# Kernel optimization log

Hardware: AMD Instinct MI355X
Metric: run time of the kernel (lower is better)

## Reference

```python
import jax, jax.numpy as jnp
import numpy as np

N = 100000
E = 3200000
FIRE, WEA, TER = 8, 12, 10
H = 64


def setup_inputs() -> dict:
    key = jax.random.key(0)
    ks = jax.random.split(key, 24)
    def lin(kw, fan_in, fan_out):
        # torch nn.Linear default init: U(-1/sqrt(fan_in), 1/sqrt(fan_in))
        b = 1.0 / np.sqrt(fan_in)
        W = jax.random.uniform(kw, (fan_in, fan_out), jnp.float32, -b, b)
        return W
    inp = {
        'x_fire': jax.random.normal(ks[0], (N, FIRE), jnp.float32),
        'x_weather': jax.random.normal(ks[1], (N, WEA), jnp.float32),
        'x_terrain': jax.random.normal(ks[2], (N, TER), jnp.float32),
        'edge_index': jax.random.randint(ks[3], (2, E), 0, N, jnp.int64),
        # modality encoders
        'w_fire': lin(ks[4], FIRE, H), 'b_fire': jnp.zeros((H,), jnp.float32),
        'w_wea': lin(ks[5], WEA, H),  'b_wea': jnp.zeros((H,), jnp.float32),
        'w_ter': lin(ks[6], TER, H),  'b_ter': jnp.zeros((H,), jnp.float32),
        # GCN layers (concat fusion -> first layer in_dim = 3H)
        'gcn_w0': lin(ks[7], 3 * H, H), 'gcn_b0': jnp.zeros((H,), jnp.float32),
        'gcn_w1': lin(ks[8], H, H),     'gcn_b1': jnp.zeros((H,), jnp.float32),
        'gcn_w2': lin(ks[9], H, H),     'gcn_b2': jnp.zeros((H,), jnp.float32),
        # output MLP: H -> H//2 -> 1
        'out_w1': lin(ks[10], H, H // 2), 'out_b1': jnp.zeros((H // 2,), jnp.float32),
        'out_w2': lin(ks[11], H // 2, 1), 'out_b2': jnp.zeros((1,), jnp.float32),
    }
    return inp


def _gcn_conv(x, src, dst, W, b):
    """PyG GCNConv: h = W x; out[i] = sum_{j->i} norm_ij h[j] + self-loop + bias,
    with norm_ij = deg[i]^-1/2 * deg[j]^-1/2, deg including the added self-loop."""
    h = x @ W                                             # [N, H]
    deg = jnp.zeros((N,), h.dtype).at[dst].add(1.0) + 1.0  # +1 self-loop
    dinv = jax.lax.rsqrt(deg)                             # deg^-0.5
    norm = dinv[src] * dinv[dst]                          # [E]
    agg = jnp.zeros_like(h).at[dst].add(h[src] * norm[:, None])
    agg = agg + h * (dinv * dinv)[:, None]                # self-loop contribution
    return agg + b


def reference(x_fire, x_weather, x_terrain, edge_index,
              w_fire, b_fire, w_wea, b_wea, w_ter, b_ter,
              gcn_w0, gcn_b0, gcn_w1, gcn_b1, gcn_w2, gcn_b2,
              out_w1, out_b1, out_w2, out_b2):
    # modality encoders (eval mode: dropout is identity)
    h_fire = jax.nn.relu(x_fire @ w_fire + b_fire)
    h_wea = jax.nn.relu(x_weather @ w_wea + b_wea)
    h_ter = jax.nn.relu(x_terrain @ w_ter + b_ter)
    x = jnp.concatenate([h_fire, h_wea, h_ter], axis=1)   # [N, 3H]
    src, dst = edge_index[0], edge_index[1]
    x = jax.nn.relu(_gcn_conv(x, src, dst, gcn_w0, gcn_b0))
    x = jax.nn.relu(_gcn_conv(x, src, dst, gcn_w1, gcn_b1))
    x = jax.nn.relu(_gcn_conv(x, src, dst, gcn_w2, gcn_b2))
    out = jax.nn.relu(x @ out_w1 + out_b1) @ out_w2 + out_b2
    return out
```

## Files before the change

### kernel.cpp

```cpp
#include <hip/hip_runtime.h>

#define NN 100000
#define NE 3200000
#define HD 64

#define NBUCK 256
#define BWID 392
#define SLACK 20480
#define COLCAP 13568
#define OVFCAP 512
#define CAP 16
#define P1_EPB 2048
#define P1_GRID ((NE + P1_EPB - 1) / P1_EPB)

typedef int      v4i __attribute__((ext_vector_type(4)));
typedef int      v2i __attribute__((ext_vector_type(2)));
typedef _Float16 h4f __attribute__((ext_vector_type(4)));

__device__ __forceinline__ void fma4(float4& a, float s, const float4& b) {
    a.x = fmaf(s, b.x, a.x); a.y = fmaf(s, b.y, a.y);
    a.z = fmaf(s, b.z, a.z); a.w = fmaf(s, b.w, a.w);
}
__device__ __forceinline__ void addh4(float4& a, const h4f& b) {
    a.x += (float)b[0]; a.y += (float)b[1]; a.z += (float)b[2]; a.w += (float)b[3];
}

__global__ void __launch_bounds__(256) partition_kernel(
    const int* __restrict__ src, const int* __restrict__ dst,
    int* __restrict__ bctl, v2i* __restrict__ pairs, v2i* __restrict__ povf) {
    __shared__ v2i stage[NBUCK][CAP];
    __shared__ int cnt[NBUCK];
    int t = threadIdx.x;
    cnt[t] = 0;
    __syncthreads();
    const v4i* d4p = (const v4i*)dst;
    const v4i* s4p = (const v4i*)src;
    const int NE4 = NE / 4;
    int base4 = blockIdx.x * (P1_EPB / 4);
    #pragma unroll
    for (int it = 0; it < P1_EPB / 1024; it++) {
        int i = base4 + it * 256 + t;
        v4i d4 = (v4i){-1, -1, -1, -1};
        v4i s4 = (v4i){0, 0, 0, 0};
        if (i < NE4) {
            d4 = __builtin_nontemporal_load(d4p + i);
            s4 = __builtin_nontemporal_load(s4p + i);
        }
        #pragma unroll
        for (int k = 0; k < 4; k++) {
            int d = d4[k];
            if (d >= 0) {
                int b = (unsigned)d / BWID;
                int slot = atomicAdd(&cnt[b], 1);
                v2i p; p[0] = s4[k]; p[1] = d;
                if (slot < CAP) {
                    stage[b][slot] = p;
                } else {
                    int o = atomicAdd(&bctl[b * 16 + 2], 1);
                    if (o < OVFCAP) povf[(size_t)b * OVFCAP + o] = p;
                }
            }
        }
    }
    __syncthreads();
    int c_tot = cnt[t];
    int c = (c_tot > CAP) ? CAP : c_tot;
    int runs = (c + 7) >> 3;
    if (runs) {
        int slots = runs * 8;
        for (int m = c; m < slots; m++) { v2i p; p[0] = 0; p[1] = -1; stage[t][m] = p; }
        int gb = atomicAdd(&bctl[t * 16], slots);
        if (gb + slots <= SLACK) {
            v4i* gp = (v4i*)(pairs + (size_t)t * SLACK + gb);
            const v4i* sp = (const v4i*)&stage[t][0];
            #pragma unroll
            for (int m = 0; m < 8; m++) { if (m < runs * 4) gp[m] = sp[m]; }
        } else {
            for (int m = 0; m < slots && gb + m < SLACK; m++)
                pairs[(size_t)t * SLACK + gb + m] = stage[t][m];
        }
    }
    if (c_tot > 0) atomicAdd(&bctl[t * 16 + 1], c_tot);
}

__global__ void bucket_scan_kernel(const int* __restrict__ bctl,
                                   int* __restrict__ bbase, int* __restrict__ rowptr) {
    __shared__ int s[NBUCK];
    int t = threadIdx.x;
    int v = bctl[t * 16 + 1];
    s[t] = v; __syncthreads();
    for (int off = 1; off < NBUCK; off <<= 1) {
        int x = (t >= off) ? s[t - off] : 0;
        __syncthreads();
        s[t] += x;
        __syncthreads();
    }
    bbase[t] = s[t] - v;
    if (t == NBUCK - 1) rowptr[NN] = s[t];
}

__global__ void __launch_bounds__(256) csr_fill_kernel(
    const v2i* __restrict__ pairs, const v2i* __restrict__ povf,
    const int* __restrict__ bctl, const int* __restrict__ bbase,
    int* __restrict__ rowptr, float* __restrict__ dinv, int* __restrict__ col) {
    __shared__ int hist[BWID];
    __shared__ int rp[BWID];
    __shared__ int cur[BWID];
    __shared__ int sc[256];
    __shared__ int cols[COLCAP];
    int b = blockIdx.x, t = threadIdx.x;
    int lo = b * BWID;
    int hi = min(lo + BWID, NN);
    int nw = hi - lo;
    for (int i = t; i < BWID; i += 256) { hist[i] = 0; cur[i] = 0; }
    __syncthreads();
    int np = bctl[b * 16];     if (np > SLACK) np = SLACK;
    int nov = bctl[b * 16 + 2]; if (nov > OVFCAP) nov = OVFCAP;
    int base = bbase[b];
    const v2i* pb = pairs + (size_t)b * SLACK;
    const v2i* ob = povf + (size_t)b * OVFCAP;
    for (int i = t; i < np; i += 256) {
        v2i p = pb[i];
        if (p[1] >= 0) atomicAdd(&hist[p[1] - lo], 1);
    }
    for (int i = t; i < nov; i += 256) {
        v2i p = ob[i];
        atomicAdd(&hist[p[1] - lo], 1);
    }
    __syncthreads();
    int h0 = 0, s2 = 0;
    if (2 * t < BWID) {
        h0 = hist[2 * t];
        int h1 = (2 * t + 1 < BWID) ? hist[2 * t + 1] : 0;
        s2 = h0 + h1;
    }
    sc[t] = s2; __syncthreads();
    for (int off = 1; off < 256; off <<= 1) {
        int x = (t >= off) ? sc[t - off] : 0;
        __syncthreads();
        sc[t] += x;
        __syncthreads();
    }
    if (2 * t < BWID) {
        int ex = sc[t] - s2;
        rp[2 * t] = ex;
        if (2 * t + 1 < BWID) rp[2 * t + 1] = ex + h0;
    }
    __syncthreads();
    for (int i = t; i < nw; i += 256) {
        rowptr[lo + i] = base + rp[i];
        dinv[lo + i] = 1.0f / sqrtf((float)(hist[i] + 1));
    }
    for (int i = t; i < np; i += 256) {
        v2i p = pb[i];
        if (p[1] >= 0) {
            int li = p[1] - lo;
            int slot = atomicAdd(&cur[li], 1);
            int o = rp[li] + slot;
            if (o < COLCAP) cols[o] = p[0];
        }
    }
    for (int i = t; i < nov; i += 256) {
        v2i p = ob[i];
        int li = p[1] - lo;
        int slot = atomicAdd(&cur[li], 1);
        int o = rp[li] + slot;
        if (o < COLCAP) cols[o] = p[0];
    }
    __syncthreads();
    int nreal = bctl[b * 16 + 1]; if (nreal > COLCAP) nreal = COLCAP;
    for (int i = t; i < nreal; i += 256)
        col[base + i] = cols[i];
}

__global__ void __launch_bounds__(256) encmm0_kernel(
    const float* __restrict__ xf, const float* __restrict__ xw, const float* __restrict__ xt,
    const float* __restrict__ Wf, const float* __restrict__ bf,
    const float* __restrict__ Ww, const float* __restrict__ bw,
    const float* __restrict__ Wt, const float* __restrict__ bt,
    const float* __restrict__ W0, const float* __restrict__ dinv,
    _Float16* __restrict__ h) {
    __shared__ float xin[64][32];
    __shared__ float wenc[30][64];
    __shared__ float bs[192];
    __shared__ float xs[64][36];
    __shared__ float ws[32][64];
    int t = threadIdx.x;
    int n0 = blockIdx.x * 64;

    {
        const float4* xf4 = (const float4*)xf;
        for (int i = t; i < 128; i += 256) {
            int n = i >> 1, q = i & 1;
            int gn = n0 + n;
            float4 v = make_float4(0, 0, 0, 0);
            if (gn < NN) v = xf4[(size_t)gn * 2 + q];
            *(float4*)&xin[n][q * 4] = v;
        }
        const float4* xw4 = (const float4*)xw;
        for (int i = t; i < 192; i += 256) {
            int n = i / 3, q = i - n * 3;
            int gn = n0 + n;
            float4 v = make_float4(0, 0, 0, 0);
            if (gn < NN) v = xw4[(size_t)gn * 3 + q];
            *(float4*)&xin[n][8 + q * 4] = v;
        }
        const float2* xt2 = (const float2*)xt;
        for (int i = t; i < 320; i += 256) {
            int n = i / 5, q = i - n * 5;
            int gn = n0 + n;
            float2 v = make_float2(0, 0);
            if (gn < NN) v = xt2[(size_t)gn * 5 + q];
            *(float2*)&xin[n][20 + q * 2] = v;
        }
        for (int i = t; i < 480; i += 256) {
            int r = i >> 4, q = i & 15;
            float4 v;
            if (r < 8)       v = ((const float4*)Wf)[r * 16 + q];
            else if (r < 20) v = ((const float4*)Ww)[(r - 8) * 16 + q];
            else             v = ((const float4*)Wt)[(r - 20) * 16 + q];
            *(float4*)&wenc[r][q * 4] = v;
        }
        if (t < 192) bs[t] = (t < 64) ? bf[t] : (t < 128) ? bw[t - 64] : bt[t - 128];
    }

    int cg = t & 15, ng = t >> 4;
    int c0 = cg * 4;
    float4 acc[4];
    #pragma unroll
    for (int i = 0; i < 4; i++) acc[i] = make_float4(0, 0, 0, 0);

    for (int kq = 0; kq < 6; kq++) {
        __syncthreads();
        {
            const float4* W04 = (const float4*)W0;
            float4* ws4 = (float4*)&ws[0][0];
            for (int i = t; i < 512; i += 256)
                ws4[i] = W04[(size_t)kq * 512 + i];
        }
        int coff = (kq < 2) ? kq * 32 : (kq < 4) ? (kq - 2) * 32 : (kq - 4) * 32;
        if (kq < 2) {
            for (int i = t; i < 2048; i += 256) {
                int n = i >> 5, kk = i & 31;
                float a = bs[kq * 32 + kk];
                #pragma unroll
                for (int k = 0; k < 8; k++) a = fmaf(xin[n][k], wenc[k][coff + kk], a);
                xs[n][kk] = fmaxf(a, 0.f);
            }
        } else if (kq < 4) {
            for (int i = t; i < 2048; i += 256) {
                int n = i >> 5, kk = i & 31;
                float a = bs[kq * 32 + kk];
                #pragma unroll
                for (int k = 0; k < 12; k++) a = fmaf(xin[n][8 + k], wenc[8 + k][coff + kk], a);
                xs[n][kk] = fmaxf(a, 0.f);
            }
        } else {
            for (int i = t; i < 2048; i += 256) {
                int n = i >> 5, kk = i & 31;
                float a = bs[kq * 32 + kk];
                #pragma unroll
                for (int k = 0; k < 10; k++) a = fmaf(xin[n][20 + k], wenc[20 + k][coff + kk], a);
                xs[n][kk] = fmaxf(a, 0.f);
            }
        }
        __syncthreads();
        for (int k = 0; k < 32; k += 4) {
            float4 b0 = *(const float4*)&ws[k + 0][c0];
            float4 b1 = *(const float4*)&ws[k + 1][c0];
            float4 b2 = *(const float4*)&ws[k + 2][c0];
            float4 b3 = *(const float4*)&ws[k + 3][c0];
            #pragma unroll
            for (int i = 0; i < 4; i++) {
                float4 a = *(const float4*)&xs[ng * 4 + i][k];
                fma4(acc[i], a.x, b0); fma4(acc[i], a.y, b1);
                fma4(acc[i], a.z, b2); fma4(acc[i], a.w, b3);
            }
        }
    }
    h4f* h4 = (h4f*)h;
    #pragma unroll
    for (int i = 0; i < 4; i++) {
        int gn = n0 + ng * 4 + i;
        if (gn < NN) {
            float dn = dinv[gn];
            h4f v;
            v[0] = (_Float16)(acc[i].x * dn);
            v[1] = (_Float16)(acc[i].y * dn);
            v[2] = (_Float16)(acc[i].z * dn);
            v[3] = (_Float16)(acc[i].w * dn);
            h4[(size_t)gn * 16 + cg] = v;
        }
    }
}

__global__ void gather_mm_kernel(
    const int* __restrict__ col, const int* __restrict__ rowptr,
    const float* __restrict__ dinv, const _Float16* __restrict__ h,
    const float* __restrict__ bias, const float* __restrict__ W,
    _Float16* __restrict__ hout) {
    int t = threadIdx.x;
    int n = (blockIdx.x * 256 + t) >> 6;
    int l = t & 63;
    if (n >= NN) return;
    int g = l >> 4;
    int q = l & 15;
    const h4f* h4 = (const h4f*)h;
    float4 acc = make_float4(0, 0, 0, 0);
    int r0 = rowptr[n], r1 = rowptr[n + 1];
    for (int base = r0; base < r1; base += 64) {
        int cnt = min(64, r1 - base);
        int pv = NN;
        if (l < cnt) pv = __builtin_nontemporal_load(col + base + l);
        int steps = (cnt + 3) >> 2;
        int j = 0;
        for (; j + 4 <= steps; j += 4) {
            int e0 = (j + 0) * 4 + g, e1 = (j + 1) * 4 + g;
            int e2 = (j + 2) * 4 + g, e3 = (j + 3) * 4 + g;
            int s0 = __shfl(pv, e0);
            int s1 = __shfl(pv, e1);
            int s2 = __shfl(pv, e2);
            int s3 = __shfl(pv, e3);
            h4f v0 = h4[(size_t)s0 * 16 + q];
            h4f v1 = h4[(size_t)s1 * 16 + q];
            h4f v2 = h4[(size_t)s2 * 16 + q];
            h4f v3 = h4[(size_t)s3 * 16 + q];
            addh4(acc, v0); addh4(acc, v1);
            addh4(acc, v2); addh4(acc, v3);
        }
        for (; j < steps; j++) {
            int e = j * 4 + g;
            int s = __shfl(pv, e);
            h4f v = h4[(size_t)s * 16 + q];
            addh4(acc, v);
        }
    }
    acc.x += __shfl_xor(acc.x, 16); acc.y += __shfl_xor(acc.y, 16);
    acc.z += __shfl_xor(acc.z, 16); acc.w += __shfl_xor(acc.w, 16);
    acc.x += __shfl_xor(acc.x, 32); acc.y += __shfl_xor(acc.y, 32);
    acc.z += __shfl_xor(acc.z, 32); acc.w += __shfl_xor(acc.w, 32);
    float dn = dinv[n];
    h4f hnh = h4[(size_t)n * 16 + q];
    float4 b4 = ((const float4*)bias)[q];
    float4 r;
    r.x = fmaxf(fmaf(dn, acc.x + (float)hnh[0], b4.x), 0.f);
    r.y = fmaxf(fmaf(dn, acc.y + (float)hnh[1], b4.y), 0.f);
    r.z = fmaxf(fmaf(dn, acc.z + (float)hnh[2], b4.z), 0.f);
    r.w = fmaxf(fmaf(dn, acc.w + (float)hnh[3], b4.w), 0.f);
    float oc0 = 0.f, oc1 = 0.f, oc2 = 0.f, oc3 = 0.f;
    #pragma unroll
    for (int qq = 0; qq < 16; qq++) {
        float rx = __shfl(r.x, qq);
        float ry = __shfl(r.y, qq);
        float rz = __shfl(r.z, qq);
        float rw = __shfl(r.w, qq);
        oc0 = fmaf(rx, W[(qq * 4 + 0) * 64 + l], oc0);
        oc1 = fmaf(ry, W[(qq * 4 + 1) * 64 + l], oc1);
        oc2 = fmaf(rz, W[(qq * 4 + 2) * 64 + l], oc2);
        oc3 = fmaf(rw, W[(qq * 4 + 3) * 64 + l], oc3);
    }
    float oc = (oc0 + oc1) + (oc2 + oc3);
    __builtin_nontemporal_store((_Float16)(oc * dn), &hout[(size_t)n * 64 + l]);
}

__global__ void gather_mlp_kernel(
    const int* __restrict__ col, const int* __restrict__ rowptr,
    const float* __restrict__ dinv, const _Float16* __restrict__ h,
    const float* __restrict__ bias, const float* __restrict__ w1,
    const float* __restrict__ b1, const float* __restrict__ w2,
    const float* __restrict__ b2, float* __restrict__ out) {
    int t = threadIdx.x;
    int n = (blockIdx.x * 256 + t) >> 6;
    int l = t & 63;
    if (n >= NN) return;
    int g = l >> 4;
    int q = l & 15;
    const h4f* h4 = (const h4f*)h;
    float4 acc = make_float4(0, 0, 0, 0);
    int r0 = rowptr[n], r1 = rowptr[n + 1];
    for (int base = r0; base < r1; base += 64) {
        int cnt = min(64, r1 - base);
        int pv = NN;
        if (l < cnt) pv = __builtin_nontemporal_load(col + base + l);
        int steps = (cnt + 3) >> 2;
        int j = 0;
        for (; j + 4 <= steps; j += 4) {
            int e0 = (j + 0) * 4 + g, e1 = (j + 1) * 4 + g;
            int e2 = (j + 2) * 4 + g, e3 = (j + 3) * 4 + g;
            int s0 = __shfl(pv, e0);
            int s1 = __shfl(pv, e1);
            int s2 = __shfl(pv, e2);
            int s3 = __shfl(pv, e3);
            h4f v0 = h4[(size_t)s0 * 16 + q];
            h4f v1 = h4[(size_t)s1 * 16 + q];
            h4f v2 = h4[(size_t)s2 * 16 + q];
            h4f v3 = h4[(size_t)s3 * 16 + q];
            addh4(acc, v0); addh4(acc, v1);
            addh4(acc, v2); addh4(acc, v3);
        }
        for (; j < steps; j++) {
            int e = j * 4 + g;
            int s = __shfl(pv, e);
            h4f v = h4[(size_t)s * 16 + q];
            addh4(acc, v);
        }
    }
    acc.x += __shfl_xor(acc.x, 16); acc.y += __shfl_xor(acc.y, 16);
    acc.z += __shfl_xor(acc.z, 16); acc.w += __shfl_xor(acc.w, 16);
    acc.x += __shfl_xor(acc.x, 32); acc.y += __shfl_xor(acc.y, 32);
    acc.z += __shfl_xor(acc.z, 32); acc.w += __shfl_xor(acc.w, 32);
    float dn = dinv[n];
    h4f hnh = h4[(size_t)n * 16 + q];
    float4 b4 = ((const float4*)bias)[q];
    float4 r;
    r.x = fmaxf(fmaf(dn, acc.x + (float)hnh[0], b4.x), 0.f);
    r.y = fmaxf(fmaf(dn, acc.y + (float)hnh[1], b4.y), 0.f);
    r.z = fmaxf(fmaf(dn, acc.z + (float)hnh[2], b4.z), 0.f);
    r.w = fmaxf(fmaf(dn, acc.w + (float)hnh[3], b4.w), 0.f);
    int c = l & 31;
    float a0 = b1[c], a1 = 0.f, a2p = 0.f, a3 = 0.f;
    #pragma unroll
    for (int qq = 0; qq < 16; qq++) {
        float rx = __shfl(r.x, qq);
        float ry = __shfl(r.y, qq);
        float rz = __shfl(r.z, qq);
        float rw = __shfl(r.w, qq);
        a0  = fmaf(rx, w1[(qq * 4 + 0) * 32 + c], a0);
        a1  = fmaf(ry, w1[(qq * 4 + 1) * 32 + c], a1);
        a2p = fmaf(rz, w1[(qq * 4 + 2) * 32 + c], a2p);
        a3  = fmaf(rw, w1[(qq * 4 + 3) * 32 + c], a3);
    }
    float a = (a0 + a1) + (a2p + a3);
    float v = fmaxf(a, 0.f) * w2[c];
    v += __shfl_xor(v, 1); v += __shfl_xor(v, 2);
    v += __shfl_xor(v, 4); v += __shfl_xor(v, 8);
    v += __shfl_xor(v, 16);
    if (l == 0) __builtin_nontemporal_store(v + b2[0], &out[n]);
}

extern "C" void kernel_launch(void* const* d_in, const int* in_sizes, int n_in,
                              void* d_out, int out_size, void* d_ws, size_t ws_size,
                              hipStream_t stream) {
    const float* xf = (const float*)d_in[0];
    const float* xw = (const float*)d_in[1];
    const float* xt = (const float*)d_in[2];
    const int*   ei = (const int*)d_in[3];
    const int*   src = ei;
    const int*   dst = ei + NE;
    const float* Wf = (const float*)d_in[4];
    const float* bf = (const float*)d_in[5];
    const float* Ww = (const float*)d_in[6];
    const float* bw = (const float*)d_in[7];
    const float* Wt = (const float*)d_in[8];
    const float* bt = (const float*)d_in[9];
    const float* W0 = (const float*)d_in[10];
    const float* b0 = (const float*)d_in[11];
    const float* W1 = (const float*)d_in[12];
    const float* b1 = (const float*)d_in[13];
    const float* W2 = (const float*)d_in[14];
    const float* b2 = (const float*)d_in[15];
    const float* ow1 = (const float*)d_in[16];
    const float* ob1 = (const float*)d_in[17];
    const float* ow2 = (const float*)d_in[18];
    const float* ob2 = (const float*)d_in[19];
    float* out = (float*)d_out;

    char* w = (char*)d_ws;
    _Float16* hA  = (_Float16*)w;  w += (size_t)(NN + 1) * 64 * 2;
    _Float16* hB  = (_Float16*)w;  w += (size_t)(NN + 1) * 64 * 2;
    int*   col    = (int*)w;    w += (size_t)NE * 4;
    v2i*   pairs  = (v2i*)w;    w += (size_t)NBUCK * SLACK * 8;
    v2i*   povf   = (v2i*)w;    w += (size_t)NBUCK * OVFCAP * 8;
    float* dinv   = (float*)w;  w += (size_t)NN * 4;
    int*   rowptr = (int*)w;    w += (size_t)(NN + 1) * 4;
    int*   bctl   = (int*)w;    w += (size_t)NBUCK * 16 * 4;
    int*   bbase  = (int*)w;    w += (size_t)NBUCK * 4;

    hipMemsetAsync(bctl, 0, (size_t)NBUCK * 16 * 4, stream);
    hipMemsetAsync(hA + (size_t)NN * 64, 0, 64 * 2, stream);
    hipMemsetAsync(hB + (size_t)NN * 64, 0, 64 * 2, stream);
    partition_kernel<<<P1_GRID, 256, 0, stream>>>(src, dst, bctl, pairs, povf);
    bucket_scan_kernel<<<1, NBUCK, 0, stream>>>(bctl, bbase, rowptr);
    csr_fill_kernel<<<NBUCK, 256, 0, stream>>>(pairs, povf, bctl, bbase, rowptr, dinv, col);

    encmm0_kernel<<<(NN + 63) / 64, 256, 0, stream>>>(xf, xw, xt, Wf, bf, Ww, bw, Wt, bt, W0, dinv, hA);
    gather_mm_kernel<<<(NN * 64 + 255) / 256, 256, 0, stream>>>(col, rowptr, dinv, hA, b0, W1, hB);
    gather_mm_kernel<<<(NN * 64 + 255) / 256, 256, 0, stream>>>(col, rowptr, dinv, hB, b1, W2, hA);
    gather_mlp_kernel<<<(NN * 64 + 255) / 256, 256, 0, stream>>>(col, rowptr, dinv, hA, b2, ow1, ob1, ow2, ob2, out);
}
```

Before: 576.7 us.

## Pack edge pairs into 32-bit words, fold bucket scan, widen gathers to 16B

Edge pairs staged by the partition kernel are packed into one 32-bit word (17-bit source, 9-bit local row), which halves the pairs buffer traffic. The staging capacity rises to 24 per bucket. The bucket prefix scan and the two halo memsets move into csr_fill, removing one kernel launch and two memset calls. The gather kernels now use 8-half (16-byte) loads per lane with 8 edges per step instead of 4, and use 32-bit index math. The packing relies on node ids fitting in 17 bits, and each csr_fill block now repeats the 256-entry scan redundantly.

```diff
diff --git a/kernel.cpp b/kernel.cpp
--- a/kernel.cpp
+++ b/kernel.cpp
@@ -9,26 +9,25 @@
 #define SLACK 20480
 #define COLCAP 13568
 #define OVFCAP 512
-#define CAP 16
+#define CAP 24
 #define P1_EPB 2048
 #define P1_GRID ((NE + P1_EPB - 1) / P1_EPB)
+#define PSENT 0xFFFFFFFFu
 
 typedef int      v4i __attribute__((ext_vector_type(4)));
 typedef int      v2i __attribute__((ext_vector_type(2)));
 typedef _Float16 h4f __attribute__((ext_vector_type(4)));
+typedef _Float16 h8f __attribute__((ext_vector_type(8)));
 
 __device__ __forceinline__ void fma4(float4& a, float s, const float4& b) {
     a.x = fmaf(s, b.x, a.x); a.y = fmaf(s, b.y, a.y);
     a.z = fmaf(s, b.z, a.z); a.w = fmaf(s, b.w, a.w);
 }
-__device__ __forceinline__ void addh4(float4& a, const h4f& b) {
-    a.x += (float)b[0]; a.y += (float)b[1]; a.z += (float)b[2]; a.w += (float)b[3];
-}
 
 __global__ void __launch_bounds__(256) partition_kernel(
     const int* __restrict__ src, const int* __restrict__ dst,
-    int* __restrict__ bctl, v2i* __restrict__ pairs, v2i* __restrict__ povf) {
-    __shared__ v2i stage[NBUCK][CAP];
+    int* __restrict__ bctl, unsigned* __restrict__ pairs, v2i* __restrict__ povf) {
+    __shared__ unsigned stage[NBUCK][CAP];
     __shared__ int cnt[NBUCK];
     int t = threadIdx.x;
     cnt[t] = 0;
@@ -52,11 +51,12 @@
             if (d >= 0) {
                 int b = (unsigned)d / BWID;
                 int slot = atomicAdd(&cnt[b], 1);
-                v2i p; p[0] = s4[k]; p[1] = d;
+                unsigned u = (unsigned)s4[k] | ((unsigned)(d - b * BWID) << 17);
                 if (slot < CAP) {
-                    stage[b][slot] = p;
+                    stage[b][slot] = u;
                 } else {
                     int o = atomicAdd(&bctl[b * 16 + 2], 1);
+                    v2i p; p[0] = s4[k]; p[1] = d;
                     if (o < OVFCAP) povf[(size_t)b * OVFCAP + o] = p;
                 }
             }
@@ -68,13 +68,13 @@
     int runs = (c + 7) >> 3;
     if (runs) {
         int slots = runs * 8;
-        for (int m = c; m < slots; m++) { v2i p; p[0] = 0; p[1] = -1; stage[t][m] = p; }
+        for (int m = c; m < slots; m++) stage[t][m] = PSENT;
         int gb = atomicAdd(&bctl[t * 16], slots);
         if (gb + slots <= SLACK) {
             v4i* gp = (v4i*)(pairs + (size_t)t * SLACK + gb);
             const v4i* sp = (const v4i*)&stage[t][0];
             #pragma unroll
-            for (int m = 0; m < 8; m++) { if (m < runs * 4) gp[m] = sp[m]; }
+            for (int m = 0; m < 6; m++) { if (m < runs * 2) gp[m] = sp[m]; }
         } else {
             for (int m = 0; m < slots && gb + m < SLACK; m++)
                 pairs[(size_t)t * SLACK + gb + m] = stage[t][m];
@@ -83,45 +83,44 @@
     if (c_tot > 0) atomicAdd(&bctl[t * 16 + 1], c_tot);
 }
 
-__global__ void bucket_scan_kernel(const int* __restrict__ bctl,
-                                   int* __restrict__ bbase, int* __restrict__ rowptr) {
-    __shared__ int s[NBUCK];
-    int t = threadIdx.x;
-    int v = bctl[t * 16 + 1];
-    s[t] = v; __syncthreads();
-    for (int off = 1; off < NBUCK; off <<= 1) {
-        int x = (t >= off) ? s[t - off] : 0;
-        __syncthreads();
-        s[t] += x;
-        __syncthreads();
-    }
-    bbase[t] = s[t] - v;
-    if (t == NBUCK - 1) rowptr[NN] = s[t];
-}
-
 __global__ void __launch_bounds__(256) csr_fill_kernel(
-    const v2i* __restrict__ pairs, const v2i* __restrict__ povf,
-    const int* __restrict__ bctl, const int* __restrict__ bbase,
-    int* __restrict__ rowptr, float* __restrict__ dinv, int* __restrict__ col) {
+    const unsigned* __restrict__ pairs, const v2i* __restrict__ povf,
+    const int* __restrict__ bctl, int* __restrict__ rowptr,
+    float* __restrict__ dinv, int* __restrict__ col,
+    _Float16* __restrict__ hA, _Float16* __restrict__ hB) {
     __shared__ int hist[BWID];
     __shared__ int rp[BWID];
     __shared__ int cur[BWID];
     __shared__ int sc[256];
     __shared__ int cols[COLCAP];
     int b = blockIdx.x, t = threadIdx.x;
+    if (b == 0 && t < 64) {
+        hA[(size_t)NN * 64 + t] = (_Float16)0.f;
+        hB[(size_t)NN * 64 + t] = (_Float16)0.f;
+    }
     int lo = b * BWID;
     int hi = min(lo + BWID, NN);
     int nw = hi - lo;
+    int bcv = bctl[t * 16 + 1];
+    sc[t] = bcv; __syncthreads();
+    for (int off = 1; off < 256; off <<= 1) {
+        int x = (t >= off) ? sc[t - off] : 0;
+        __syncthreads();
+        sc[t] += x;
+        __syncthreads();
+    }
+    int base = (b > 0) ? sc[b - 1] : 0;
+    if (b == 0 && t == 255) rowptr[NN] = sc[255];
+    __syncthreads();
     for (int i = t; i < BWID; i += 256) { hist[i] = 0; cur[i] = 0; }
     __syncthreads();
     int np = bctl[b * 16];     if (np > SLACK) np = SLACK;
     int nov = bctl[b * 16 + 2]; if (nov > OVFCAP) nov = OVFCAP;
-    int base = bbase[b];
-    const v2i* pb = pairs + (size_t)b * SLACK;
+    const unsigned* pb = pairs + (size_t)b * SLACK;
     const v2i* ob = povf + (size_t)b * OVFCAP;
     for (int i = t; i < np; i += 256) {
-        v2i p = pb[i];
-        if (p[1] >= 0) atomicAdd(&hist[p[1] - lo], 1);
+        unsigned u = pb[i];
+        if (u != PSENT) atomicAdd(&hist[(u >> 17) & 0x1FF], 1);
     }
     for (int i = t; i < nov; i += 256) {
         v2i p = ob[i];
@@ -152,12 +151,12 @@
         dinv[lo + i] = 1.0f / sqrtf((float)(hist[i] + 1));
     }
     for (int i = t; i < np; i += 256) {
-        v2i p = pb[i];
-        if (p[1] >= 0) {
-            int li = p[1] - lo;
+        unsigned u = pb[i];
+        if (u != PSENT) {
+            int li = (u >> 17) & 0x1FF;
             int slot = atomicAdd(&cur[li], 1);
             int o = rp[li] + slot;
-            if (o < COLCAP) cols[o] = p[0];
+            if (o < COLCAP) cols[o] = (int)(u & 0x1FFFF);
         }
     }
     for (int i = t; i < nov; i += 256) {
@@ -289,9 +288,14 @@
             v[1] = (_Float16)(acc[i].y * dn);
             v[2] = (_Float16)(acc[i].z * dn);
             v[3] = (_Float16)(acc[i].w * dn);
-            h4[(size_t)gn * 16 + cg] = v;
-        }
-    }
+            h4[((unsigned)gn << 4) + cg] = v;
+        }
+    }
+}
+
+__device__ __forceinline__ void addh8(float* a, const h8f& b) {
+    #pragma unroll
+    for (int k = 0; k < 8; k++) a[k] += (float)b[k];
 }
 
 __global__ void gather_mm_kernel(
@@ -303,64 +307,75 @@
     int n = (blockIdx.x * 256 + t) >> 6;
     int l = t & 63;
     if (n >= NN) return;
-    int g = l >> 4;
-    int q = l & 15;
-    const h4f* h4 = (const h4f*)h;
-    float4 acc = make_float4(0, 0, 0, 0);
+    int g = l >> 3;
+    int q = l & 7;
+    const h8f* h8 = (const h8f*)h;
+    float dn = dinv[n];
+    h8f hnh = h8[((unsigned)n << 3) + q];
+    float4 ba = ((const float4*)bias)[q * 2];
+    float4 bb = ((const float4*)bias)[q * 2 + 1];
+    float acc[8] = {0, 0, 0, 0, 0, 0, 0, 0};
     int r0 = rowptr[n], r1 = rowptr[n + 1];
     for (int base = r0; base < r1; base += 64) {
         int cnt = min(64, r1 - base);
         int pv = NN;
         if (l < cnt) pv = __builtin_nontemporal_load(col + base + l);
-        int steps = (cnt + 3) >> 2;
+        int steps = (cnt + 7) >> 3;
         int j = 0;
         for (; j + 4 <= steps; j += 4) {
-            int e0 = (j + 0) * 4 + g, e1 = (j + 1) * 4 + g;
-            int e2 = (j + 2) * 4 + g, e3 = (j + 3) * 4 + g;
-            int s0 = __shfl(pv, e0);
-            int s1 = __shfl(pv, e1);
-            int s2 = __shfl(pv, e2);
-            int s3 = __shfl(pv, e3);
-            h4f v0 = h4[(size_t)s0 * 16 + q];
-            h4f v1 = h4[(size_t)s1 * 16 + q];
-            h4f v2 = h4[(size_t)s2 * 16 + q];
-            h4f v3 = h4[(size_t)s3 * 16 + q];
-            addh4(acc, v0); addh4(acc, v1);
-            addh4(acc, v2); addh4(acc, v3);
+            int s0 = __shfl(pv, (j + 0) * 8 + g);
+            int s1 = __shfl(pv, (j + 1) * 8 + g);
+            int s2 = __shfl(pv, (j + 2) * 8 + g);
+            int s3 = __shfl(pv, (j + 3) * 8 + g);
+            h8f v0 = h8[((unsigned)s0 << 3) + q];
+            h8f v1 = h8[((unsigned)s1 << 3) + q];
+            h8f v2 = h8[((unsigned)s2 << 3) + q];
+            h8f v3 = h8[((unsigned)s3 << 3) + q];
+            addh8(acc, v0); addh8(acc, v1); addh8(acc, v2); addh8(acc, v3);
         }
         for (; j < steps; j++) {
-            int e = j * 4 + g;
-            int s = __shfl(pv, e);
-            h4f v = h4[(size_t)s * 16 + q];
-            addh4(acc, v);
-        }
-    }
-    acc.x += __shfl_xor(acc.x, 16); acc.y += __shfl_xor(acc.y, 16);
-    acc.z += __shfl_xor(acc.z, 16); acc.w += __shfl_xor(acc.w, 16);
-    acc.x += __shfl_xor(acc.x, 32); acc.y += __shfl_xor(acc.y, 32);
-    acc.z += __shfl_xor(acc.z, 32); acc.w += __shfl_xor(acc.w, 32);
-    float dn = dinv[n];
-    h4f hnh = h4[(size_t)n * 16 + q];
-    float4 b4 = ((const float4*)bias)[q];
-    float4 r;
-    r.x = fmaxf(fmaf(dn, acc.x + (float)hnh[0], b4.x), 0.f);
-    r.y = fmaxf(fmaf(dn, acc.y + (float)hnh[1], b4.y), 0.f);
-    r.z = fmaxf(fmaf(dn, acc.z + (float)hnh[2], b4.z), 0.f);
-    r.w = fmaxf(fmaf(dn, acc.w + (float)hnh[3], b4.w), 0.f);
+            int s0 = __shfl(pv, j * 8 + g);
+            h8f v0 = h8[((unsigned)s0 << 3) + q];
+            addh8(acc, v0);
+        }
+    }
+    #pragma unroll
+    for (int k = 0; k < 8; k++) {
+        acc[k] += __shfl_xor(acc[k], 8);
+        acc[k] += __shfl_xor(acc[k], 16);
+        acc[k] += __shfl_xor(acc[k], 32);
+    }
+    float r[8];
+    r[0] = fmaxf(fmaf(dn, acc[0] + (float)hnh[0], ba.x), 0.f);
+    r[1] = fmaxf(fmaf(dn, acc[1] + (float)hnh[1], ba.y), 0.f);
+    r[2] = fmaxf(fmaf(dn, acc[2] + (float)hnh[2], ba.z), 0.f);
+    r[3] = fmaxf(fmaf(dn, acc[3] + (float)hnh[3], ba.w), 0.f);
+    r[4] = fmaxf(fmaf(dn, acc[4] + (float)hnh[4], bb.x), 0.f);
+    r[5] = fmaxf(fmaf(dn, acc[5] + (float)hnh[5], bb.y), 0.f);
+    r[6] = fmaxf(fmaf(dn, acc[6] + (float)hnh[6], bb.z), 0.f);
+    r[7] = fmaxf(fmaf(dn, acc[7] + (float)hnh[7], bb.w), 0.f);
     float oc0 = 0.f, oc1 = 0.f, oc2 = 0.f, oc3 = 0.f;
     #pragma unroll
-    for (int qq = 0; qq < 16; qq++) {
-        float rx = __shfl(r.x, qq);
-        float ry = __shfl(r.y, qq);
-        float rz = __shfl(r.z, qq);
-        float rw = __shfl(r.w, qq);
-        oc0 = fmaf(rx, W[(qq * 4 + 0) * 64 + l], oc0);
-        oc1 = fmaf(ry, W[(qq * 4 + 1) * 64 + l], oc1);
-        oc2 = fmaf(rz, W[(qq * 4 + 2) * 64 + l], oc2);
-        oc3 = fmaf(rw, W[(qq * 4 + 3) * 64 + l], oc3);
+    for (int qq = 0; qq < 8; qq++) {
+        float r0b = __shfl(r[0], qq);
+        float r1b = __shfl(r[1], qq);
+        float r2b = __shfl(r[2], qq);
+        float r3b = __shfl(r[3], qq);
+        float r4b = __shfl(r[4], qq);
+        float r5b = __shfl(r[5], qq);
+        float r6b = __shfl(r[6], qq);
+        float r7b = __shfl(r[7], qq);
+        oc0 = fmaf(r0b, W[(qq * 8 + 0) * 64 + l], oc0);
+        oc1 = fmaf(r1b, W[(qq * 8 + 1) * 64 + l], oc1);
+        oc2 = fmaf(r2b, W[(qq * 8 + 2) * 64 + l], oc2);
+        oc3 = fmaf(r3b, W[(qq * 8 + 3) * 64 + l], oc3);
+        oc0 = fmaf(r4b, W[(qq * 8 + 4) * 64 + l], oc0);
+        oc1 = fmaf(r5b, W[(qq * 8 + 5) * 64 + l], oc1);
+        oc2 = fmaf(r6b, W[(qq * 8 + 6) * 64 + l], oc2);
+        oc3 = fmaf(r7b, W[(qq * 8 + 7) * 64 + l], oc3);
     }
     float oc = (oc0 + oc1) + (oc2 + oc3);
-    __builtin_nontemporal_store((_Float16)(oc * dn), &hout[(size_t)n * 64 + l]);
+    __builtin_nontemporal_store((_Float16)(oc * dn), &hout[((unsigned)n << 6) + l]);
 }
 
 __global__ void gather_mlp_kernel(
@@ -373,62 +388,73 @@
     int n = (blockIdx.x * 256 + t) >> 6;
     int l = t & 63;
     if (n >= NN) return;
-    int g = l >> 4;
-    int q = l & 15;
-    const h4f* h4 = (const h4f*)h;
-    float4 acc = make_float4(0, 0, 0, 0);
+    int g = l >> 3;
+    int q = l & 7;
+    const h8f* h8 = (const h8f*)h;
+    float dn = dinv[n];
+    h8f hnh = h8[((unsigned)n << 3) + q];
+    float4 ba = ((const float4*)bias)[q * 2];
+    float4 bb = ((const float4*)bias)[q * 2 + 1];
+    float acc[8] = {0, 0, 0, 0, 0, 0, 0, 0};
     int r0 = rowptr[n], r1 = rowptr[n + 1];
     for (int base = r0; base < r1; base += 64) {
         int cnt = min(64, r1 - base);
         int pv = NN;
         if (l < cnt) pv = __builtin_nontemporal_load(col + base + l);
-        int steps = (cnt + 3) >> 2;
+        int steps = (cnt + 7) >> 3;
         int j = 0;
         for (; j + 4 <= steps; j += 4) {
-            int e0 = (j + 0) * 4 + g, e1 = (j + 1) * 4 + g;
-            int e2 = (j + 2) * 4 + g, e3 = (j + 3) * 4 + g;
-            int s0 = __shfl(pv, e0);
-            int s1 = __shfl(pv, e1);
-            int s2 = __shfl(pv, e2);
-            int s3 = __shfl(pv, e3);
-            h4f v0 = h4[(size_t)s0 * 16 + q];
-            h4f v1 = h4[(size_t)s1 * 16 + q];
-            h4f v2 = h4[(size_t)s2 * 16 + q];
-            h4f v3 = h4[(size_t)s3 * 16 + q];
-            addh4(acc, v0); addh4(acc, v1);
-            addh4(acc, v2); addh4(acc, v3);
+            int s0 = __shfl(pv, (j + 0) * 8 + g);
+            int s1 = __shfl(pv, (j + 1) * 8 + g);
+            int s2 = __shfl(pv, (j + 2) * 8 + g);
+            int s3 = __shfl(pv, (j + 3) * 8 + g);
+            h8f v0 = h8[((unsigned)s0 << 3) + q];
+            h8f v1 = h8[((unsigned)s1 << 3) + q];
+            h8f v2 = h8[((unsigned)s2 << 3) + q];
+            h8f v3 = h8[((unsigned)s3 << 3) + q];
+            addh8(acc, v0); addh8(acc, v1); addh8(acc, v2); addh8(acc, v3);
         }
         for (; j < steps; j++) {
-            int e = j * 4 + g;
-            int s = __shfl(pv, e);
-            h4f v = h4[(size_t)s * 16 + q];
-            addh4(acc, v);
-        }
-    }
-    acc.x += __shfl_xor(acc.x, 16); acc.y += __shfl_xor(acc.y, 16);
-    acc.z += __shfl_xor(acc.z, 16); acc.w += __shfl_xor(acc.w, 16);
-    acc.x += __shfl_xor(acc.x, 32); acc.y += __shfl_xor(acc.y, 32);
-    acc.z += __shfl_xor(acc.z, 32); acc.w += __shfl_xor(acc.w, 32);
-    float dn = dinv[n];
-    h4f hnh = h4[(size_t)n * 16 + q];
-    float4 b4 = ((const float4*)bias)[q];
-    float4 r;
-    r.x = fmaxf(fmaf(dn, acc.x + (float)hnh[0], b4.x), 0.f);
-    r.y = fmaxf(fmaf(dn, acc.y + (float)hnh[1], b4.y), 0.f);
-    r.z = fmaxf(fmaf(dn, acc.z + (float)hnh[2], b4.z), 0.f);
-    r.w = fmaxf(fmaf(dn, acc.w + (float)hnh[3], b4.w), 0.f);
+            int s0 = __shfl(pv, j * 8 + g);
+            h8f v0 = h8[((unsigned)s0 << 3) + q];
+            addh8(acc, v0);
+        }
+    }
+    #pragma unroll
+    for (int k = 0; k < 8; k++) {
+        acc[k] += __shfl_xor(acc[k], 8);
+        acc[k] += __shfl_xor(acc[k], 16);
+        acc[k] += __shfl_xor(acc[k], 32);
+    }
+    float r[8];
+    r[0] = fmaxf(fmaf(dn, acc[0] + (float)hnh[0], ba.x), 0.f);
+    r[1] = fmaxf(fmaf(dn, acc[1] + (float)hnh[1], ba.y), 0.f);
+    r[2] = fmaxf(fmaf(dn, acc[2] + (float)hnh[2], ba.z), 0.f);
+    r[3] = fmaxf(fmaf(dn, acc[3] + (float)hnh[3], ba.w), 0.f);
+    r[4] = fmaxf(fmaf(dn, acc[4] + (float)hnh[4], bb.x), 0.f);
+    r[5] = fmaxf(fmaf(dn, acc[5] + (float)hnh[5], bb.y), 0.f);
+    r[6] = fmaxf(fmaf(dn, acc[6] + (float)hnh[6], bb.z), 0.f);
+    r[7] = fmaxf(fmaf(dn, acc[7] + (float)hnh[7], bb.w), 0.f);
     int c = l & 31;
     float a0 = b1[c], a1 = 0.f, a2p = 0.f, a3 = 0.f;
     #pragma unroll
-    for (int qq = 0; qq < 16; qq++) {
-        float rx = __shfl(r.x, qq);
-        float ry = __shfl(r.y, qq);
-        float rz = __shfl(r.z, qq);
-        float rw = __shfl(r.w, qq);
-        a0  = fmaf(rx, w1[(qq * 4 + 0) * 32 + c], a0);
-        a1  = fmaf(ry, w1[(qq * 4 + 1) * 32 + c], a1);
-        a2p = fmaf(rz, w1[(qq * 4 + 2) * 32 + c], a2p);
-        a3  = fmaf(rw, w1[(qq * 4 + 3) * 32 + c], a3);
+    for (int qq = 0; qq < 8; qq++) {
+        float r0b = __shfl(r[0], qq);
+        float r1b = __shfl(r[1], qq);
+        float r2b = __shfl(r[2], qq);
+        float r3b = __shfl(r[3], qq);
+        float r4b = __shfl(r[4], qq);
+        float r5b = __shfl(r[5], qq);
+        float r6b = __shfl(r[6], qq);
+        float r7b = __shfl(r[7], qq);
+        a0  = fmaf(r0b, w1[(qq * 8 + 0) * 32 + c], a0);
+        a1  = fmaf(r1b, w1[(qq * 8 + 1) * 32 + c], a1);
+        a2p = fmaf(r2b, w1[(qq * 8 + 2) * 32 + c], a2p);
+        a3  = fmaf(r3b, w1[(qq * 8 + 3) * 32 + c], a3);
+        a0  = fmaf(r4b, w1[(qq * 8 + 4) * 32 + c], a0);
+        a1  = fmaf(r5b, w1[(qq * 8 + 5) * 32 + c], a1);
+        a2p = fmaf(r6b, w1[(qq * 8 + 6) * 32 + c], a2p);
+        a3  = fmaf(r7b, w1[(qq * 8 + 7) * 32 + c], a3);
     }
     float a = (a0 + a1) + (a2p + a3);
     float v = fmaxf(a, 0.f) * w2[c];
@@ -469,19 +495,15 @@
     _Float16* hA  = (_Float16*)w;  w += (size_t)(NN + 1) * 64 * 2;
     _Float16* hB  = (_Float16*)w;  w += (size_t)(NN + 1) * 64 * 2;
     int*   col    = (int*)w;    w += (size_t)NE * 4;
-    v2i*   pairs  = (v2i*)w;    w += (size_t)NBUCK * SLACK * 8;
+    unsigned* pairs = (unsigned*)w; w += (size_t)NBUCK * SLACK * 4;
     v2i*   povf   = (v2i*)w;    w += (size_t)NBUCK * OVFCAP * 8;
     float* dinv   = (float*)w;  w += (size_t)NN * 4;
     int*   rowptr = (int*)w;    w += (size_t)(NN + 1) * 4;
     int*   bctl   = (int*)w;    w += (size_t)NBUCK * 16 * 4;
-    int*   bbase  = (int*)w;    w += (size_t)NBUCK * 4;
 
     hipMemsetAsync(bctl, 0, (size_t)NBUCK * 16 * 4, stream);
-    hipMemsetAsync(hA + (size_t)NN * 64, 0, 64 * 2, stream);
-    hipMemsetAsync(hB + (size_t)NN * 64, 0, 64 * 2, stream);
     partition_kernel<<<P1_GRID, 256, 0, stream>>>(src, dst, bctl, pairs, povf);
-    bucket_scan_kernel<<<1, NBUCK, 0, stream>>>(bctl, bbase, rowptr);
-    csr_fill_kernel<<<NBUCK, 256, 0, stream>>>(pairs, povf, bctl, bbase, rowptr, dinv, col);
+    csr_fill_kernel<<<NBUCK, 256, 0, stream>>>(pairs, povf, bctl, rowptr, dinv, col, hA, hB);
 
     encmm0_kernel<<<(NN + 63) / 64, 256, 0, stream>>>(xf, xw, xt, Wf, bf, Ww, bw, Wt, bt, W0, dinv, hA);
     gather_mm_kernel<<<(NN * 64 + 255) / 256, 256, 0, stream>>>(col, rowptr, dinv, hA, b0, W1, hB);
```

Measured after the change: 572.4 us. About the same (-0.8%).
